# Performance work log

Hardware: AMD Instinct MI355X
Metric: run time of the kernel (lower is better)

Reference implementation:

```python
import jax, jax.numpy as jnp
import numpy as np

# Grid constants (must match fill_max of coordinate inputs)
B, T, Y, X = 2, 8, 128, 128
YO, XO = 2 * Y - 1, 2 * X - 1  # spconv transpose: (in-1)*2 - 2*1 + 3 = 2*in - 1
EPS = 1e-5


def setup_inputs() -> dict:
    key = jax.random.key(0)
    ks = jax.random.split(key, 8)
    N, CIN, COUT = 262144, 128, 64
    feats = jax.random.normal(ks[0], (N, CIN), dtype=jnp.float32)
    # kernel-offset-major weight layout [kt, ky, kx, Cin, Cout]
    weight = jax.random.normal(ks[1], (3, 3, 3, CIN, COUT), dtype=jnp.float32) * 0.05
    gamma = jnp.ones((COUT,), jnp.float32)
    beta = jnp.zeros((COUT,), jnp.float32)
    coords_b = jax.random.randint(ks[2], (N,), 0, B, dtype=jnp.int32)
    coords_t = jax.random.randint(ks[3], (N,), 0, T, dtype=jnp.int32)
    coords_y = jax.random.randint(ks[4], (N,), 0, Y, dtype=jnp.int32)
    coords_x = jax.random.randint(ks[5], (N,), 0, X, dtype=jnp.int32)
    return {"feats": feats, "weight": weight, "gamma": gamma, "beta": beta,
            "coords_b": coords_b, "coords_t": coords_t,
            "coords_y": coords_y, "coords_x": coords_x}


def _sparse_deconv(feats, weight, cb, ct, cy, cx):
    """Rulebook-style transpose conv: for each of 27 kernel offsets,
    GEMM the input features and scatter-add into the (dense) output grid.
    Output coord: out = in*stride - pad + k. Grid padded by 1 so out-of-range
    contributions land in the halo and are sliced away (equivalent to spconv
    dropping rules outside the output extent)."""
    COUT = weight.shape[-1]
    grid = jnp.zeros((B, T + 2, YO + 2, XO + 2, COUT), feats.dtype)
    cnt = jnp.zeros((B, T + 2, YO + 2, XO + 2), jnp.float32)
    ones = jnp.ones((feats.shape[0],), jnp.float32)
    for kt in range(3):
        ot = ct - 1 + kt + 1  # stride 1 in t; +1 = halo offset
        for ky in range(3):
            oy = 2 * cy - 1 + ky + 1
            for kx in range(3):
                ox = 2 * cx - 1 + kx + 1
                msg = feats @ weight[kt, ky, kx]  # [N, Cout]
                grid = grid.at[cb, ot, oy, ox].add(msg)
                cnt = cnt.at[cb, ot, oy, ox].add(ones)
    return grid[:, 1:-1, 1:-1, 1:-1], cnt[:, 1:-1, 1:-1, 1:-1]


def reference(feats, weight, gamma, beta, coords_b, coords_t, coords_y, coords_x):
    # sort_sparse_tensor only reorders voxels; math is order-invariant here.
    grid, cnt = _sparse_deconv(feats, weight, coords_b, coords_t, coords_y, coords_x)
    mask = (cnt > 0).astype(grid.dtype)  # active output sites [B,T,YO,XO]
    n = jnp.maximum(mask.sum(), 1.0)
    # BatchNorm1d over active-site features (grid is exactly 0 at inactive sites)
    mean = grid.sum(axis=(0, 1, 2, 3)) / n
    var = (grid * grid).sum(axis=(0, 1, 2, 3)) / n - mean * mean  # biased var
    rstd = jax.lax.rsqrt(var + EPS)
    out = (grid - mean) * (rstd * gamma) + beta
    out = out * mask[..., None]  # keep inactive sites at zero (sparse semantics)
    return jax.nn.relu(out)
```

## Files before the change

### kernel.cpp

```cpp
#include <hip/hip_runtime.h>
#include <hip/hip_bf16.h>

#define BB   2
#define TT   8
#define YY   128
#define XX   128
#define CINv 128
#define COUTv 64
#define YOv  255
#define XOv  255
#define NVOX 262144
#define NSITES (BB*TT*YY*XX)
#define CAP  16
#define OUT_SITES (BB*TT*YOv*XOv)
#define OUT_ELEMS ((size_t)OUT_SITES*COUTv)

typedef float  f32x4  __attribute__((ext_vector_type(4)));
typedef __bf16 bf16x8 __attribute__((ext_vector_type(8)));
typedef unsigned int u32x4 __attribute__((ext_vector_type(4)));

union FragU { u32x4 u; bf16x8 b; };
union Pack8 { unsigned short s[8]; u32x4 u; };

constexpr size_t OFF_STATS = 0;
constexpr size_t OFF_CNT   = 1024;
constexpr size_t ZERO_BYTES= OFF_CNT + 1048576;
constexpr size_t OFF_DBF   = ZERO_BYTES;
constexpr size_t OFF_PB    = OFF_DBF + 67108864;
constexpr size_t OFF_MASK  = OFF_PB + 442368;
constexpr size_t OFF_SS    = OFF_MASK + 1048576;
constexpr size_t OFF_IDX   = OFF_SS + 1024;
constexpr size_t OFF_OUTB  = OFF_IDX;

__device__ __forceinline__ unsigned short f2bf(float f) {
    unsigned u = __float_as_uint(f);
    u += 0x7fffu + ((u >> 16) & 1u);
    return (unsigned short)(u >> 16);
}

__device__ __forceinline__ void gld16(const void* g, void* l) {
    __builtin_amdgcn_global_load_lds(
        (const __attribute__((address_space(1))) unsigned int*)g,
        (__attribute__((address_space(3))) unsigned int*)l, 16, 0, 0);
}

__global__ __launch_bounds__(256) void k_count(
    const int* __restrict__ cb, const int* __restrict__ ct,
    const int* __restrict__ cy, const int* __restrict__ cx,
    unsigned int* __restrict__ cnt, int* __restrict__ idx)
{
    int n = blockIdx.x * 256 + threadIdx.x;
    int site = ((cb[n] * TT + ct[n]) * YY + cy[n]) * XX + cx[n];
    unsigned slot = atomicAdd(cnt + site, 1u);
    if (slot < CAP) idx[site * CAP + slot] = n;
}

__global__ __launch_bounds__(256) void k_gather(
    const float* __restrict__ feats,
    const unsigned int* __restrict__ cnt, const int* __restrict__ idx,
    unsigned short* __restrict__ Dbf)
{
    int tid = blockIdx.x * 256 + threadIdx.x;
    int site = tid >> 4;
    int c8 = (tid & 15) * 8;
    unsigned c = cnt[site]; if (c > CAP) c = CAP;
    float a[8] = {0.f,0.f,0.f,0.f,0.f,0.f,0.f,0.f};
    const int* ip = idx + (size_t)site * CAP;
    if (c) {
        const int4 i4 = *(const int4*)ip;
        int nv[4] = { i4.x, i4.y, i4.z, i4.w };
        #pragma unroll
        for (int v = 0; v < 4; ++v) {
            if ((unsigned)v < c) {
                int n = nv[v];
                const float4 f0 = *(const float4*)(feats + (size_t)n * CINv + c8);
                const float4 f1 = *(const float4*)(feats + (size_t)n * CINv + c8 + 4);
                a[0] += f0.x; a[1] += f0.y; a[2] += f0.z; a[3] += f0.w;
                a[4] += f1.x; a[5] += f1.y; a[6] += f1.z; a[7] += f1.w;
            }
        }
        for (unsigned v = 4; v < c; ++v) {
            int n = ip[v];
            const float4 f0 = *(const float4*)(feats + (size_t)n * CINv + c8);
            const float4 f1 = *(const float4*)(feats + (size_t)n * CINv + c8 + 4);
            a[0] += f0.x; a[1] += f0.y; a[2] += f0.z; a[3] += f0.w;
            a[4] += f1.x; a[5] += f1.y; a[6] += f1.z; a[7] += f1.w;
        }
    }
    Pack8 p;
    #pragma unroll
    for (int j = 0; j < 8; ++j) p.s[j] = f2bf(a[j]);
    *(u32x4*)(Dbf + (size_t)site * CINv + c8) = p.u;
}

__global__ __launch_bounds__(64) void k_pack(
    const float* __restrict__ W, unsigned short* __restrict__ PB)
{
    int f = blockIdx.x;
    int w  = f >> 4;
    int kc = (f >> 2) & 3;
    int nt = f & 3;
    int lane = threadIdx.x;
    int q = lane >> 4, col = lane & 15;
    Pack8 p;
    #pragma unroll
    for (int j = 0; j < 8; ++j) {
        int k  = kc * 32 + q * 8 + j;
        int nn = nt * 16 + col;
        p.s[j] = f2bf(W[((size_t)w * CINv + k) * COUTv + nn]);
    }
    *(u32x4*)(PB + ((size_t)f * 64 + lane) * 8) = p.u;
}

__global__ __launch_bounds__(256) void k_mask(
    const unsigned int* __restrict__ occ,
    unsigned char* __restrict__ mask, unsigned int* __restrict__ ncnt)
{
    int s = blockIdx.x * 256 + threadIdx.x;
    bool found = false;
    if (s < OUT_SITES) {
        int xo = s % XOv; int r = s / XOv;
        int yo = r % YOv; r /= YOv;
        int to = r & 7;   int b = r >> 3;
        int cts[3]; int ntc = 0;
        for (int kt = 0; kt < 3; ++kt) { int c = to + 1 - kt; if (c >= 0 && c < TT) cts[ntc++] = c; }
        int cys[2]; int nyc;
        if (yo & 1) { cys[0] = (yo + 1) >> 1; cys[1] = (yo - 1) >> 1; nyc = 2; }
        else        { cys[0] = yo >> 1; nyc = 1; }
        int cxs[2]; int nxc;
        if (xo & 1) { cxs[0] = (xo + 1) >> 1; cxs[1] = (xo - 1) >> 1; nxc = 2; }
        else        { cxs[0] = xo >> 1; nxc = 1; }
        for (int i = 0; i < ntc && !found; ++i)
            for (int j = 0; j < nyc && !found; ++j)
                for (int k = 0; k < nxc && !found; ++k)
                    if (occ[((b * TT + cts[i]) * YY + cys[j]) * XX + cxs[k]]) found = true;
        mask[s] = found ? 1 : 0;
    }
    unsigned long long bal = __ballot(found);
    if ((threadIdx.x & 63) == 0) {
        unsigned c = (unsigned)__popcll(bal);
        if (c) atomicAdd(ncnt, c);
    }
}


#define MFMA_BF16(A, B, C) __builtin_amdgcn_mfma_f32_16x16x32_bf16((A), (B), (C), 0, 0, 0)

#define BPASS2(bt, SLOT) do {                                                            \
    _Pragma("unroll")                                                                    \
    for (int kc = 0; kc < 4; ++kc) {                                                     \
        FragU Bf[4];                                                                     \
        _Pragma("unroll")                                                                \
        for (int nt = 0; nt < 4; ++nt)                                                   \
            Bf[nt].u = *(const u32x4*)((bt) + (size_t)((kc * 4 + nt) * 64 + lane) * 8);  \
        _Pragma("unroll")                                                                \
        for (int nt = 0; nt < 4; ++nt) {                                                 \
            acc0[SLOT][nt]     = MFMA_BF16(Aa0[kc].b, Bf[nt].b, acc0[SLOT][nt]);         \
            acc0[SLOT + 2][nt] = MFMA_BF16(Ab0[kc].b, Bf[nt].b, acc0[SLOT + 2][nt]);     \
            acc1[SLOT][nt]     = MFMA_BF16(Aa1[kc].b, Bf[nt].b, acc1[SLOT][nt]);         \
            acc1[SLOT + 2][nt] = MFMA_BF16(Ab1[kc].b, Bf[nt].b, acc1[SLOT + 2][nt]);     \
        }                                                                                \
    } } while (0)

__global__ __launch_bounds__(256, 2) void k_conv(
    const unsigned short* __restrict__ Dbf,
    const unsigned short* __restrict__ PB,
    unsigned short* __restrict__ outb,
    float* __restrict__ gsum, float* __restrict__ gsq)
{
    const int lane = threadIdx.x & 63;
    const int wave = threadIdx.x >> 6;
    const int bid = blockIdx.x;

    const int xcd  = bid & 7;
    const int u    = bid >> 3;
    const int band = u >> 2;
    const int tl   = (u >> 1) & 1;
    const int par  = u & 1;
    const int b    = xcd >> 2;
    const int to   = (xcd & 3) * 2 + tl;
    const int yo0  = 4 * band + par;
    const bool has2 = (yo0 + 2 <= 254);

    const int m = lane & 15, q = lane >> 4;

    __shared__ __align__(16) unsigned short shB[3 * 16 * 64 * 8];
    __shared__ float shsum[64], shsq[64];
    if (threadIdx.x < 64) { shsum[threadIdx.x] = 0.f; shsq[threadIdx.x] = 0.f; }

    int ycy[2], yky[2], ny;
    if ((yo0 & 1) == 0) { ny = 1; ycy[0] = yo0 >> 1; yky[0] = 1; }
    else { ny = 2; ycy[0] = (yo0 + 1) >> 1; yky[0] = 0; ycy[1] = (yo0 - 1) >> 1; yky[1] = 2; }

    f32x4 acc0[4][4], acc1[4][4];
    #pragma unroll
    for (int ch = 0; ch < 4; ++ch)
        #pragma unroll
        for (int nt = 0; nt < 4; ++nt) {
            acc0[ch][nt] = (f32x4){0.f, 0.f, 0.f, 0.f};
            acc1[ch][nt] = (f32x4){0.f, 0.f, 0.f, 0.f};
        }

    for (int kt = 0; kt < 3; ++kt) {
        int ct = to + 1 - kt;
        if (ct < 0 || ct >= TT) continue;
        for (int iy = 0; iy < ny; ++iy) {
            __syncthreads();
            {
                const char* gsrc = (const char*)PB + (size_t)((kt * 3 + yky[iy]) * 3) * 16384;
                char* ldst = (char*)shB;
                #pragma unroll
                for (int r = 0; r < 12; ++r)
                    gld16(gsrc + r * 4096 + threadIdx.x * 16,
                          ldst + r * 4096 + wave * 1024);
            }
            int cy0 = ycy[iy];
            int cy1 = has2 ? cy0 + 1 : cy0;
            size_t plane0 = ((size_t)((b * TT + ct) * YY + cy0)) * XX;
            size_t plane1 = ((size_t)((b * TT + ct) * YY + cy1)) * XX;
            FragU Aa0[4], Ab0[4], Aa1[4], Ab1[4];
            {
                const unsigned short* pa0 = Dbf + (plane0 + (size_t)(2 * wave * 16 + m)) * CINv;
                const unsigned short* pb0 = Dbf + (plane0 + (size_t)((2 * wave + 1) * 16 + m)) * CINv;
                const unsigned short* pa1 = Dbf + (plane1 + (size_t)(2 * wave * 16 + m)) * CINv;
                const unsigned short* pb1 = Dbf + (plane1 + (size_t)((2 * wave + 1) * 16 + m)) * CINv;
                #pragma unroll
                for (int kc = 0; kc < 4; ++kc) {
                    Aa0[kc].u = *(const u32x4*)(pa0 + kc * 32 + q * 8);
                    Ab0[kc].u = *(const u32x4*)(pb0 + kc * 32 + q * 8);
                    Aa1[kc].u = *(const u32x4*)(pa1 + kc * 32 + q * 8);
                    Ab1[kc].u = *(const u32x4*)(pb1 + kc * 32 + q * 8);
                }
            }
            __syncthreads();

            BPASS2(shB + 8192,  0);
            BPASS2(shB + 16384, 1);

            {
                int cxb1 = (2 * wave + 1) * 16 + m + 1; if (cxb1 > 127) cxb1 = 127;
                const unsigned short* pa0 = Dbf + (plane0 + (size_t)(2 * wave * 16 + m + 1)) * CINv;
                const unsigned short* pb0 = Dbf + (plane0 + (size_t)cxb1) * CINv;
                const unsigned short* pa1 = Dbf + (plane1 + (size_t)(2 * wave * 16 + m + 1)) * CINv;
                const unsigned short* pb1 = Dbf + (plane1 + (size_t)cxb1) * CINv;
                #pragma unroll
                for (int kc = 0; kc < 4; ++kc) {
                    Aa0[kc].u = *(const u32x4*)(pa0 + kc * 32 + q * 8);
                    Ab0[kc].u = *(const u32x4*)(pb0 + kc * 32 + q * 8);
                    Aa1[kc].u = *(const u32x4*)(pa1 + kc * 32 + q * 8);
                    Ab1[kc].u = *(const u32x4*)(pb1 + kc * 32 + q * 8);
                }
            }
            BPASS2(shB + 0, 1);
        }
    }

    float sl[4] = {0.f,0.f,0.f,0.f}, sq[4] = {0.f,0.f,0.f,0.f};
    {
        size_t rowbase = ((size_t)((b * TT + to) * YOv + yo0)) * XOv;
        #pragma unroll
        for (int ch = 0; ch < 4; ++ch) {
            int cb8 = 2 * wave + (ch >> 1);
            int px = ch & 1;
            #pragma unroll
            for (int nt = 0; nt < 4; ++nt) {
                int c = nt * 16 + m;
                #pragma unroll
                for (int i = 0; i < 4; ++i) {
                    int r = q * 4 + i;
                    int xo = 2 * (cb8 * 16 + r) + px;
                    if (xo < XOv) {
                        float v = acc0[ch][nt][i];
                        outb[(rowbase + xo) * COUTv + c] = f2bf(v);
                        sl[nt] += v; sq[nt] += v * v;
                    }
                }
            }
        }
    }
    if (has2) {
        size_t rowbase = ((size_t)((b * TT + to) * YOv + (yo0 + 2))) * XOv;
        #pragma unroll
        for (int ch = 0; ch < 4; ++ch) {
            int cb8 = 2 * wave + (ch >> 1);
            int px = ch & 1;
            #pragma unroll
            for (int nt = 0; nt < 4; ++nt) {
                int c = nt * 16 + m;
                #pragma unroll
                for (int i = 0; i < 4; ++i) {
                    int r = q * 4 + i;
                    int xo = 2 * (cb8 * 16 + r) + px;
                    if (xo < XOv) {
                        float v = acc1[ch][nt][i];
                        outb[(rowbase + xo) * COUTv + c] = f2bf(v);
                        sl[nt] += v; sq[nt] += v * v;
                    }
                }
            }
        }
    }
    #pragma unroll
    for (int nt = 0; nt < 4; ++nt) {
        sl[nt] += __shfl_xor(sl[nt], 16); sl[nt] += __shfl_xor(sl[nt], 32);
        sq[nt] += __shfl_xor(sq[nt], 16); sq[nt] += __shfl_xor(sq[nt], 32);
    }
    if (lane < 16) {
        #pragma unroll
        for (int nt = 0; nt < 4; ++nt) {
            atomicAdd(&shsum[nt * 16 + lane], sl[nt]);
            atomicAdd(&shsq [nt * 16 + lane], sq[nt]);
        }
    }
    __syncthreads();
    if (threadIdx.x < 64) {
        unsafeAtomicAdd(&gsum[threadIdx.x], shsum[threadIdx.x]);
        unsafeAtomicAdd(&gsq [threadIdx.x], shsq [threadIdx.x]);
    }
}

__global__ __launch_bounds__(64) void k_final(
    const float* __restrict__ gsum, const float* __restrict__ gsq,
    const unsigned int* __restrict__ ncnt,
    const float* __restrict__ gamma, const float* __restrict__ beta,
    float* __restrict__ scale, float* __restrict__ shift)
{
    int c = threadIdx.x;
    float nf = (float)max(*ncnt, 1u);
    float mean = gsum[c] / nf;
    float var  = gsq[c] / nf - mean * mean;
    float rstd = rsqrtf(var + 1e-5f);
    float sc = rstd * gamma[c];
    scale[c] = sc;
    shift[c] = beta[c] - mean * sc;
}

__global__ __launch_bounds__(256) void k_norm(
    const unsigned short* __restrict__ outb, float* __restrict__ out,
    const unsigned char* __restrict__ mask,
    const float* __restrict__ scale, const float* __restrict__ shift)
{
    __shared__ float ssc[64], ssh[64];
    if (threadIdx.x < 64) { ssc[threadIdx.x] = scale[threadIdx.x]; ssh[threadIdx.x] = shift[threadIdx.x]; }
    __syncthreads();
    size_t t = (size_t)blockIdx.x * 256 + threadIdx.x;
    size_t e = t * 8;
    if (e >= OUT_ELEMS) return;
    Pack8 p; p.u = *(const u32x4*)(outb + e);
    int c = (int)(e & 63);
    size_t site = e >> 6;
    float4 v0, v1;
    if (mask[site]) {
        float w[8];
        #pragma unroll
        for (int j = 0; j < 8; ++j) {
            float f = __uint_as_float((unsigned)p.s[j] << 16);
            w[j] = fmaxf(fmaf(f, ssc[c + j], ssh[c + j]), 0.f);
        }
        v0 = make_float4(w[0], w[1], w[2], w[3]);
        v1 = make_float4(w[4], w[5], w[6], w[7]);
    } else {
        v0 = make_float4(0.f, 0.f, 0.f, 0.f);
        v1 = v0;
    }
    *(float4*)(out + e) = v0;
    *(float4*)(out + e + 4) = v1;
}

extern "C" void kernel_launch(void* const* d_in, const int* in_sizes, int n_in,
                              void* d_out, int out_size, void* d_ws, size_t ws_size,
                              hipStream_t stream)
{
    const float* feats = (const float*)d_in[0];
    const float* W     = (const float*)d_in[1];
    const float* gamma = (const float*)d_in[2];
    const float* beta  = (const float*)d_in[3];
    const int* cb = (const int*)d_in[4];
    const int* ct = (const int*)d_in[5];
    const int* cy = (const int*)d_in[6];
    const int* cx = (const int*)d_in[7];
    float* out = (float*)d_out;

    char* ws = (char*)d_ws;
    float*          gsum = (float*)(ws + OFF_STATS);
    float*          gsq  = gsum + 64;
    unsigned int*   ncnt = (unsigned int*)(ws + OFF_STATS + 512);
    unsigned int*   cnt  = (unsigned int*)(ws + OFF_CNT);
    unsigned short* Dbf  = (unsigned short*)(ws + OFF_DBF);
    unsigned short* PB   = (unsigned short*)(ws + OFF_PB);
    unsigned char*  mask = (unsigned char*)(ws + OFF_MASK);
    float*          scale= (float*)(ws + OFF_SS);
    float*          shift= scale + 64;
    int*            idx  = (int*)(ws + OFF_IDX);
    unsigned short* outb = (unsigned short*)(ws + OFF_OUTB);

    hipMemsetAsync(d_ws, 0, ZERO_BYTES, stream);

    k_count<<<NVOX / 256, 256, 0, stream>>>(cb, ct, cy, cx, cnt, idx);
    k_gather<<<NSITES * 16 / 256, 256, 0, stream>>>(feats, cnt, idx, Dbf);
    k_pack<<<27 * 16, 64, 0, stream>>>(W, PB);
    k_mask<<<(OUT_SITES + 255) / 256, 256, 0, stream>>>(cnt, mask, ncnt);
    k_conv<<<2048, 256, 0, stream>>>(Dbf, PB, outb, gsum, gsq);
    k_final<<<1, 64, 0, stream>>>(gsum, gsq, ncnt, gamma, beta, scale, shift);
    k_norm<<<(int)((OUT_ELEMS / 8 + 255) / 256), 256, 0, stream>>>(outb, out, mask, scale, shift);
}
```

Before: 868.0 us.

## Remap conv blocks per XCD, raise occupancy hint, fold BN finalize into norm

Changes the k_conv block-to-work mapping so each XCD gets a contiguous span of y-bands across all (b,t) pairs instead of fixed (b,t) slices, with the aim of better L2 locality for shared input rows. It raises the launch-bounds occupancy hint from 2 to 3 blocks per CU, which limits registers and risks spills given the large accumulator arrays. It also removes the single-block k_final launch by computing scale and shift inside every k_norm block. That saves one launch at the cost of redundant per-block stat reads.

```diff
diff --git a/kernel.cpp b/kernel.cpp
--- a/kernel.cpp
+++ b/kernel.cpp
@@ -162,7 +162,7 @@
         }                                                                                \
     } } while (0)
 
-__global__ __launch_bounds__(256, 2) void k_conv(
+__global__ __launch_bounds__(256, 3) void k_conv(
     const unsigned short* __restrict__ Dbf,
     const unsigned short* __restrict__ PB,
     unsigned short* __restrict__ outb,
@@ -174,12 +174,11 @@
 
     const int xcd  = bid & 7;
     const int u    = bid >> 3;
-    const int band = u >> 2;
-    const int tl   = (u >> 1) & 1;
-    const int par  = u & 1;
-    const int b    = xcd >> 2;
-    const int to   = (xcd & 3) * 2 + tl;
-    const int yo0  = 4 * band + par;
+    const int bt   = u & 15;
+    const int b    = bt >> 3;
+    const int to   = bt & 7;
+    const int v    = xcd * 16 + (u >> 4);
+    const int yo0  = 4 * (v >> 1) + (v & 1);
     const bool has2 = (yo0 + 2 <= 254);
 
     const int m = lane & 15, q = lane >> 4;
@@ -270,9 +269,9 @@
                     int r = q * 4 + i;
                     int xo = 2 * (cb8 * 16 + r) + px;
                     if (xo < XOv) {
-                        float v = acc0[ch][nt][i];
-                        outb[(rowbase + xo) * COUTv + c] = f2bf(v);
-                        sl[nt] += v; sq[nt] += v * v;
+                        float v2 = acc0[ch][nt][i];
+                        outb[(rowbase + xo) * COUTv + c] = f2bf(v2);
+                        sl[nt] += v2; sq[nt] += v2 * v2;
                     }
                 }
             }
@@ -292,9 +291,9 @@
                     int r = q * 4 + i;
                     int xo = 2 * (cb8 * 16 + r) + px;
                     if (xo < XOv) {
-                        float v = acc1[ch][nt][i];
-                        outb[(rowbase + xo) * COUTv + c] = f2bf(v);
-                        sl[nt] += v; sq[nt] += v * v;
+                        float v2 = acc1[ch][nt][i];
+                        outb[(rowbase + xo) * COUTv + c] = f2bf(v2);
+                        sl[nt] += v2; sq[nt] += v2 * v2;
                     }
                 }
             }
@@ -319,29 +318,24 @@
     }
 }
 
-__global__ __launch_bounds__(64) void k_final(
-    const float* __restrict__ gsum, const float* __restrict__ gsq,
-    const unsigned int* __restrict__ ncnt,
-    const float* __restrict__ gamma, const float* __restrict__ beta,
-    float* __restrict__ scale, float* __restrict__ shift)
-{
-    int c = threadIdx.x;
-    float nf = (float)max(*ncnt, 1u);
-    float mean = gsum[c] / nf;
-    float var  = gsq[c] / nf - mean * mean;
-    float rstd = rsqrtf(var + 1e-5f);
-    float sc = rstd * gamma[c];
-    scale[c] = sc;
-    shift[c] = beta[c] - mean * sc;
-}
-
 __global__ __launch_bounds__(256) void k_norm(
     const unsigned short* __restrict__ outb, float* __restrict__ out,
     const unsigned char* __restrict__ mask,
-    const float* __restrict__ scale, const float* __restrict__ shift)
+    const float* __restrict__ gsum, const float* __restrict__ gsq,
+    const unsigned int* __restrict__ ncnt,
+    const float* __restrict__ gamma, const float* __restrict__ beta)
 {
     __shared__ float ssc[64], ssh[64];
-    if (threadIdx.x < 64) { ssc[threadIdx.x] = scale[threadIdx.x]; ssh[threadIdx.x] = shift[threadIdx.x]; }
+    if (threadIdx.x < 64) {
+        int c = threadIdx.x;
+        float nf = (float)max(*ncnt, 1u);
+        float mean = gsum[c] / nf;
+        float var  = gsq[c] / nf - mean * mean;
+        float rstd = rsqrtf(var + 1e-5f);
+        float sc = rstd * gamma[c];
+        ssc[c] = sc;
+        ssh[c] = beta[c] - mean * sc;
+    }
     __syncthreads();
     size_t t = (size_t)blockIdx.x * 256 + threadIdx.x;
     size_t e = t * 8;
@@ -389,8 +383,6 @@
     unsigned short* Dbf  = (unsigned short*)(ws + OFF_DBF);
     unsigned short* PB   = (unsigned short*)(ws + OFF_PB);
     unsigned char*  mask = (unsigned char*)(ws + OFF_MASK);
-    float*          scale= (float*)(ws + OFF_SS);
-    float*          shift= scale + 64;
     int*            idx  = (int*)(ws + OFF_IDX);
     unsigned short* outb = (unsigned short*)(ws + OFF_OUTB);
 
@@ -401,6 +393,6 @@
     k_pack<<<27 * 16, 64, 0, stream>>>(W, PB);
     k_mask<<<(OUT_SITES + 255) / 256, 256, 0, stream>>>(cnt, mask, ncnt);
     k_conv<<<2048, 256, 0, stream>>>(Dbf, PB, outb, gsum, gsq);
-    k_final<<<1, 64, 0, stream>>>(gsum, gsq, ncnt, gamma, beta, scale, shift);
-    k_norm<<<(int)((OUT_ELEMS / 8 + 255) / 256), 256, 0, stream>>>(outb, out, mask, scale, shift);
-}
+    k_norm<<<(int)((OUT_ELEMS / 8 + 255) / 256), 256, 0, stream>>>(
+        outb, out, mask, gsum, gsq, ncnt, gamma, beta);
+}
```

Result: slower. 1.109 ms (+27.7%).
